# Kernel tuning notes

Measured on AMD Instinct MI355X. Metric: run time of the kernel, lower is better.

## Reference

```python
import jax, jax.numpy as jnp
import numpy as np
from jax.scipy.special import logsumexp

NEG = -1e30  # stand-in for -inf that is safe under fp32 and vjp
MAX_SEG_LEN = 64
WITH_TRANSITION = True


def setup_inputs() -> dict:
    key = jax.random.key(0)
    k1, k2 = jax.random.split(key)
    B, S, L = 8, 512, 32
    segment_score = jax.random.normal(k1, (B, S, S, L), dtype=jnp.float32)
    transitions = jax.random.uniform(k2, (L, L), dtype=jnp.float32)  # matches nn.init.uniform_(0,1)
    return {"segment_score": segment_score, "transitions": transitions}


def _compute_log_z(segment_score, transitions, max_seg_len=MAX_SEG_LEN, with_transition=WITH_TRANSITION):
    # segment_score: [B, S, S, L] (start, end, label); transitions: [L, L]
    B, S, _, L = segment_score.shape
    M = max_seg_len
    dt = segment_score.dtype
    diag = jnp.diagonal(transitions)  # [L]

    # alpha_pad slot (p + M) holds log_alpha at frame p; slots < M act as -inf guard
    alpha_pad = jnp.full((B, S + M, L), NEG, dtype=dt)
    alpha_pad = alpha_pad.at[:, M, :].set(segment_score[:, 0, 0, :])

    w = jnp.arange(M)
    j = (M - w).astype(dt)  # window slot w corresponds to segment length j = M - w
    # transition term for a continuation segment of length j ending in label cur, coming from prev:
    # T[prev, cur] + diag[cur] * (j - 1)   -> [M, prev, cur]
    trans_term = transitions[None, :, :] + diag[None, None, :] * (j[:, None, None] - 1.0)

    def step(alpha_pad, f_end):
        # segment scores for all segments ending at f_end: [B, S, L]
        seg_col = jax.lax.dynamic_index_in_dim(segment_score, f_end, axis=2, keepdims=False)
        # pad so window slot w maps to start position f_end - M + 1 + w (length j = M - w)
        seg_pad = jnp.pad(seg_col, ((0, 0), (M - 1, 0), (0, 0)))
        seg_win = jax.lax.dynamic_slice_in_dim(seg_pad, f_end, M, axis=1)     # [B, M, L]
        # alpha window slot w -> frame f_end - M + w = f_end - j (guarded by NEG padding)
        alpha_win = jax.lax.dynamic_slice_in_dim(alpha_pad, f_end, M, axis=1)  # [B, M, L]

        # continuation scores: alpha[prev] + seg * j (+ transition)  -> [B, M, prev, cur]
        scores = alpha_win[:, :, :, None] + (seg_win * j[None, :, None])[:, :, None, :]
        if with_transition:
            scores = scores + trans_term[None, :, :, :]

        # initial segment [0, f_end] (no predecessor), only valid while f_end + 1 <= M
        f = f_end.astype(dt)
        init = seg_col[:, 0, :] * (f + 1.0)
        if with_transition:
            init = init + diag[None, :] * f
        init = jnp.where(f_end < M, init, NEG)

        all_scores = jnp.concatenate([scores.reshape(B, M * L, L), init[:, None, :]], axis=1)
        new_alpha = logsumexp(all_scores, axis=1)  # [B, L]

        alpha_pad = jax.lax.dynamic_update_slice_in_dim(
            alpha_pad, new_alpha[:, None, :], f_end + M, axis=1)
        return alpha_pad, None

    alpha_pad, _ = jax.lax.scan(step, alpha_pad, jnp.arange(1, S))
    log_z = logsumexp(alpha_pad[:, S - 1 + M, :], axis=1)  # [B]
    return log_z


def reference(segment_score, transitions):
    return _compute_log_z(segment_score, transitions)
```

## Files before the change

### kernel.cpp

```cpp
#include <hip/hip_runtime.h>

#define NEGF (-1e30f)

constexpr int S = 512;
constexpr int L = 32;


template <int CTRL>
__device__ __forceinline__ float dppf(float x) {
    return __builtin_bit_cast(float,
        __builtin_amdgcn_update_dpp(0, __builtin_bit_cast(int, x),
                                    CTRL, 0xf, 0xf, true));
}
#define GR8_MAX(v) do { v = fmaxf(v, dppf<0xB1>(v));    \
                        v = fmaxf(v, dppf<0x4E>(v));    \
                        v = fmaxf(v, dppf<0x141>(v)); } while (0)
#define GR8_ADD(v) do { v += dppf<0xB1>(v);                        \
                        v += dppf<0x4E>(v);                        \
                        v += dppf<0x141>(v); } while (0)

#define PREFETCH(dst, fe_) do {                                              \
    int fe2 = (fe_); if (fe2 > S - 1) fe2 = S - 1;                           \
    _Pragma("unroll")                                                        \
    for (int i = 0; i < 8; ++i) {                                            \
        const int j0 = jg * 8 + i + 1;                                       \
        int st = fe2 - j0 + 1; st = st < 0 ? 0 : st;                         \
        dst[i] = segB[((size_t)st * S + fe2) * L];                           \
    }                                                                        \
} while (0)

#define PHASE2(p_) do {                                                      \
    const int p_v = (p_);                                                    \
    const float4 a4 = *(const float4*)&alpha[p_v & 1][jg * 4];               \
    float mx = fmaxf(fmaxf(a4.x, a4.y), fmaxf(a4.z, a4.w));                  \
    GR8_MAX(mx);                                                             \
    float sb = __expf(a4.x - mx) * E0 + __expf(a4.y - mx) * E1               \
             + __expf(a4.z - mx) * E2 + __expf(a4.w - mx) * E3;              \
    GR8_ADD(sb);                                                             \
    if (jg == 0) ring[(p_v & 63) * 33 + cur] = mx + __logf(sb);              \
} while (0)

#define STEP(fe_, sv, EARLY) do {                                           \
    const int fe_v = (fe_);                                                 \
    float term[8];                                                          \
    _Pragma("unroll")                                                       \
    for (int i = 0; i < 8; ++i) {                                           \
        const int j0 = jg * 8 + i + 1;                                      \
        const float base = fmaf(sv[i], (float)j0, diag_c * (float)(j0 - 1));\
        float tv;                                                           \
        if (EARLY) {                                                        \
            tv = NEGF;                                                      \
            if (j0 <= fe_v)          tv = ring[((fe_v - j0) & 63) * 33 + cur] + base; \
            else if (j0 == fe_v + 1) tv = base;                             \
        } else {                                                            \
            tv = ring[((fe_v - j0) & 63) * 33 + cur] + base;                \
        }                                                                   \
        term[i] = tv;                                                       \
    }                                                                       \
    float M = fmaxf(fmaxf(fmaxf(term[0], term[1]), fmaxf(term[2], term[3])),\
                    fmaxf(fmaxf(term[4], term[5]), fmaxf(term[6], term[7])));\
    GR8_MAX(M);                                                             \
    float ss = ((__expf(term[0] - M) + __expf(term[1] - M)) +               \
                (__expf(term[2] - M) + __expf(term[3] - M))) +              \
               ((__expf(term[4] - M) + __expf(term[5] - M)) +               \
                (__expf(term[6] - M) + __expf(term[7] - M)));               \
    GR8_ADD(ss);                                                            \
    if (jg == 0) alpha[fe_v & 1][cur] = M + __logf(ss);                     \
    __syncthreads();                                                        \
    PHASE2(fe_v);                                                           \
} while (0)

__launch_bounds__(256, 1)
__global__ void semicrf_fwd(const float* __restrict__ seg,
                            const float* __restrict__ trans,
                            float* __restrict__ out)
{
    const int t   = threadIdx.x;
    const int b   = blockIdx.x;
    const int cur = t >> 3;
    const int jg  = t & 7;

    __shared__ float ring[64 * 33];
    __shared__ float alpha[2][32];

    const float diag_c = trans[cur * 33];
    const float E0 = __expf(trans[(jg * 4 + 0) * 32 + cur]);
    const float E1 = __expf(trans[(jg * 4 + 1) * 32 + cur]);
    const float E2 = __expf(trans[(jg * 4 + 2) * 32 + cur]);
    const float E3 = __expf(trans[(jg * 4 + 3) * 32 + cur]);

    if (t < 32)
        alpha[0][t] = seg[(size_t)b * S * S * L + t];
    __syncthreads();
    PHASE2(0);

    const float* segB = seg + (size_t)b * S * S * L + cur;

    float svA[8], svB[8];
    PREFETCH(svA, 1);

    for (int fe = 1; fe <= 63; fe += 2) {
        PREFETCH(svB, fe + 1);
        STEP(fe, svA, true);
        PREFETCH(svA, fe + 2);
        STEP(fe + 1, svB, true);
    }
    for (int fe = 65; fe <= 509; fe += 2) {
        PREFETCH(svB, fe + 1);
        STEP(fe, svA, false);
        PREFETCH(svA, fe + 2);
        STEP(fe + 1, svB, false);
    }
    STEP(511, svA, false);

    if (t < 64) {
        float v  = (t < 32) ? alpha[1][t] : NEGF;
        float m  = v;
        float ss = 1.f;
        #pragma unroll
        for (int mk = 1; mk <= 32; mk <<= 1) {
            const float m2 = __shfl_xor(m, mk);
            const float s2 = __shfl_xor(ss, mk);
            const float mn = fmaxf(m, m2);
            ss = ss * __expf(m - mn) + s2 * __expf(m2 - mn);
            m  = mn;
        }
        if (t == 0) out[b] = m + __logf(ss);
    }
}

extern "C" void kernel_launch(void* const* d_in, const int* in_sizes, int n_in,
                              void* d_out, int out_size, void* d_ws, size_t ws_size,
                              hipStream_t stream) {
    const float* seg   = (const float*)d_in[0];
    const float* trans = (const float*)d_in[1];
    float* out = (float*)d_out;
    hipLaunchKernelGGL(semicrf_fwd, dim3(8), dim3(256), 0, stream,
                       seg, trans, out);
}
```

Measured before the change: 696.7 us.

## Deepen segment-score prefetch to two steps and use LDS-only barrier

Rotates four register buffers so the global loads of segment scores are issued two recurrence steps ahead instead of one. This hides more of the memory latency behind the serial logsumexp chain. It also replaces __syncthreads with a barrier fenced only on workgroup-local memory, so outstanding global loads need not be drained at each step. The cost is more registers and reliance on the narrower fence being enough for correctness.

```diff
diff --git a/kernel.cpp b/kernel.cpp
--- a/kernel.cpp
+++ b/kernel.cpp
@@ -15,29 +15,35 @@
 #define GR8_MAX(v) do { v = fmaxf(v, dppf<0xB1>(v));    \
                         v = fmaxf(v, dppf<0x4E>(v));    \
                         v = fmaxf(v, dppf<0x141>(v)); } while (0)
-#define GR8_ADD(v) do { v += dppf<0xB1>(v);                        \
-                        v += dppf<0x4E>(v);                        \
+#define GR8_ADD(v) do { v += dppf<0xB1>(v);                                 \
+                        v += dppf<0x4E>(v);                                 \
                         v += dppf<0x141>(v); } while (0)
 
-#define PREFETCH(dst, fe_) do {                                              \
-    int fe2 = (fe_); if (fe2 > S - 1) fe2 = S - 1;                           \
-    _Pragma("unroll")                                                        \
-    for (int i = 0; i < 8; ++i) {                                            \
-        const int j0 = jg * 8 + i + 1;                                       \
-        int st = fe2 - j0 + 1; st = st < 0 ? 0 : st;                         \
-        dst[i] = segB[((size_t)st * S + fe2) * L];                           \
-    }                                                                        \
+#define LDS_BARRIER() do {                                                  \
+    __builtin_amdgcn_fence(__ATOMIC_RELEASE, "workgroup", "local");         \
+    __builtin_amdgcn_s_barrier();                                           \
+    __builtin_amdgcn_fence(__ATOMIC_ACQUIRE, "workgroup", "local");         \
 } while (0)
 
-#define PHASE2(p_) do {                                                      \
-    const int p_v = (p_);                                                    \
-    const float4 a4 = *(const float4*)&alpha[p_v & 1][jg * 4];               \
-    float mx = fmaxf(fmaxf(a4.x, a4.y), fmaxf(a4.z, a4.w));                  \
-    GR8_MAX(mx);                                                             \
-    float sb = __expf(a4.x - mx) * E0 + __expf(a4.y - mx) * E1               \
-             + __expf(a4.z - mx) * E2 + __expf(a4.w - mx) * E3;              \
-    GR8_ADD(sb);                                                             \
-    if (jg == 0) ring[(p_v & 63) * 33 + cur] = mx + __logf(sb);              \
+#define PREFETCH(dst, fe_) do {                                             \
+    int fe2 = (fe_); if (fe2 > S - 1) fe2 = S - 1;                          \
+    _Pragma("unroll")                                                       \
+    for (int i = 0; i < 8; ++i) {                                           \
+        const int j0 = jg * 8 + i + 1;                                      \
+        int st = fe2 - j0 + 1; st = st < 0 ? 0 : st;                        \
+        dst[i] = segB[((size_t)st * S + fe2) * L];                          \
+    }                                                                       \
+} while (0)
+
+#define PHASE2(p_) do {                                                     \
+    const int p_v = (p_);                                                   \
+    const float4 a4 = *(const float4*)&alpha[p_v & 1][jg * 4];              \
+    float mx = fmaxf(fmaxf(a4.x, a4.y), fmaxf(a4.z, a4.w));                 \
+    GR8_MAX(mx);                                                            \
+    float sb = __expf(a4.x - mx) * E0 + __expf(a4.y - mx) * E1              \
+             + __expf(a4.z - mx) * E2 + __expf(a4.w - mx) * E3;             \
+    GR8_ADD(sb);                                                            \
+    if (jg == 0) ring[(p_v & 63) * 33 + cur] = mx + __logf(sb);             \
 } while (0)
 
 #define STEP(fe_, sv, EARLY) do {                                           \
@@ -66,7 +72,7 @@
                 (__expf(term[6] - M) + __expf(term[7] - M)));               \
     GR8_ADD(ss);                                                            \
     if (jg == 0) alpha[fe_v & 1][cur] = M + __logf(ss);                     \
-    __syncthreads();                                                        \
+    LDS_BARRIER();                                                          \
     PHASE2(fe_v);                                                           \
 } while (0)
 
@@ -96,22 +102,26 @@
 
     const float* segB = seg + (size_t)b * S * S * L + cur;
 
-    float svA[8], svB[8];
-    PREFETCH(svA, 1);
+    float sv0[8], sv1[8], sv2[8], sv3[8];
+    PREFETCH(sv0, 1);
+    PREFETCH(sv1, 2);
 
-    for (int fe = 1; fe <= 63; fe += 2) {
-        PREFETCH(svB, fe + 1);
-        STEP(fe, svA, true);
-        PREFETCH(svA, fe + 2);
-        STEP(fe + 1, svB, true);
+    for (int fe = 1; fe <= 61; fe += 4) {
+        PREFETCH(sv2, fe + 2); STEP(fe + 0, sv0, true);
+        PREFETCH(sv3, fe + 3); STEP(fe + 1, sv1, true);
+        PREFETCH(sv0, fe + 4); STEP(fe + 2, sv2, true);
+        PREFETCH(sv1, fe + 5); STEP(fe + 3, sv3, true);
     }
-    for (int fe = 65; fe <= 509; fe += 2) {
-        PREFETCH(svB, fe + 1);
-        STEP(fe, svA, false);
-        PREFETCH(svA, fe + 2);
-        STEP(fe + 1, svB, false);
+    for (int fe = 65; fe <= 505; fe += 4) {
+        PREFETCH(sv2, fe + 2); STEP(fe + 0, sv0, false);
+        PREFETCH(sv3, fe + 3); STEP(fe + 1, sv1, false);
+        PREFETCH(sv0, fe + 4); STEP(fe + 2, sv2, false);
+        PREFETCH(sv1, fe + 5); STEP(fe + 3, sv3, false);
     }
-    STEP(511, svA, false);
+    PREFETCH(sv2, 511);
+    STEP(509, sv0, false);
+    STEP(510, sv1, false);
+    STEP(511, sv2, false);
 
     if (t < 64) {
         float v  = (t < 32) ? alpha[1][t] : NEGF;
```

After: 693.2 us. About the same (-0.5%).
